# Kernel optimization log

Measured on AMD Instinct MI355X. Metric: run time of the kernel, lower is better.

## Reference

```python
import jax, jax.numpy as jnp
import numpy as np

INP = 512
HIDDEN = 512
N_HEADS = 8          # called 'head_dim' in the torch code
D_HEAD = HIDDEN // N_HEADS  # 64
BASE = 10000.0
SCALE = D_HEAD ** (-0.5)


def rope(x):
    # x: [b, s, h, d]
    b, s, h, d = x.shape
    half = d // 2
    theta = 1.0 / (BASE ** (jnp.arange(0, d, 2, dtype=jnp.float32) / d))  # [d/2]
    idx_theta = jnp.arange(s, dtype=jnp.float32)[:, None] * theta[None, :]  # [s, d/2]
    idx_theta2 = jnp.concatenate([idx_theta, idx_theta], axis=1)            # [s, d]
    neg_half = jnp.concatenate([-x[..., half:], x[..., :half]], axis=-1)
    cos = jnp.cos(idx_theta2)[None, :, None, :]
    sin = jnp.sin(idx_theta2)[None, :, None, :]
    return x * cos + neg_half * sin


def setup_inputs() -> dict:
    key = jax.random.key(0)
    ks = jax.random.split(key, 10)
    b, s = 4, 2048
    init = lambda k, shp, fan_in: jax.random.normal(k, shp, jnp.float32) * (fan_in ** -0.5)
    return {
        "x": jax.random.normal(ks[0], (b, s, INP), jnp.float32),
        "c": jax.random.normal(ks[1], (b, s, INP), jnp.float32),
        "Wq": init(ks[2], (INP, HIDDEN), INP), "bq": jnp.zeros((HIDDEN,), jnp.float32),
        "Wk": init(ks[3], (INP, HIDDEN), INP), "bk": jnp.zeros((HIDDEN,), jnp.float32),
        "Wv": init(ks[4], (INP, HIDDEN), INP), "bv": jnp.zeros((HIDDEN,), jnp.float32),
        "Wo": init(ks[5], (HIDDEN, INP), HIDDEN), "bo": jnp.zeros((INP,), jnp.float32),
    }


def reference(x, c, Wq, bq, Wk, bk, Wv, bv, Wo, bo):
    b, s, _ = x.shape
    h_res = x
    q = (c @ Wq + bq).reshape(b, s, N_HEADS, D_HEAD)
    k = (x @ Wk + bk).reshape(b, s, N_HEADS, D_HEAD)
    v = (x @ Wv + bv).reshape(b, s, N_HEADS, D_HEAD)
    q = rope(q)
    k = rope(k)  # computed but unused, exactly as in the source
    # NOTE: source computes scores between q and V (not k) -- faithful reproduction
    att = jnp.einsum('bihd,bjhd->bhij', q, v)            # [b, h, s, s]
    att = jax.nn.softmax(att * SCALE, axis=-1)
    out = jnp.einsum('bhij,bjhd->bihd', att, v)          # [b, s, h, d]
    out = out.reshape(b, s, HIDDEN)
    out = out @ Wo + bo
    return out + h_res
```

## Files before the change

### kernel.cpp

```cpp
#include <hip/hip_runtime.h>
#include <hip/hip_bf16.h>
#include <cstdint>

typedef float f32x4 __attribute__((ext_vector_type(4)));
typedef short bf16x8 __attribute__((ext_vector_type(8)));
typedef short bf16x4 __attribute__((ext_vector_type(4)));
typedef unsigned short u16;

#define B_    4
#define S_    2048
#define H_    8
#define D_    64
#define M_    8192

#define OFF_CBF   0UL
#define OFF_XBF   8388608UL
#define OFF_QBH   16777216UL
#define OFF_VBH   25165824UL
#define OFF_VTBH  33554432UL
#define OFF_ATTN  41943040UL
#define OFF_WQT   50331648UL
#define OFF_WVT   50855936UL
#define OFF_WOT   51380224UL
#define OFF_BIAS  51904512UL
#define OFF_COS   51910656UL
#define OFF_SIN   52172800UL
#define WS_NEEDED 52434944UL

__device__ __forceinline__ u16 f2bf(float f){
    union { float f; uint32_t u; } v; v.f = f;
    uint32_t r = (v.u + 0x7fffu + ((v.u >> 16) & 1u)) >> 16;
    return (u16)r;
}
__device__ __forceinline__ float bf2f(u16 h){
    union { uint32_t u; float f; } v; v.u = ((uint32_t)h) << 16;
    return v.f;
}
__device__ __forceinline__ uint32_t fbits(float f){
    union { float f; uint32_t u; } v; v.f = f; return v.u;
}

__device__ __forceinline__ f32x4 mfma16(bf16x4 a, bf16x4 b, f32x4 c){
#if __has_builtin(__builtin_amdgcn_mfma_f32_16x16x16bf16_1k)
    return __builtin_amdgcn_mfma_f32_16x16x16bf16_1k(a, b, c, 0, 0, 0);
#else
    asm volatile("v_mfma_f32_16x16x16_bf16 %0, %1, %2, %0" : "+v"(c) : "v"(a), "v"(b));
    return c;
#endif
}

__device__ __forceinline__ int swz(int row, int col){
    return (col & ~63) | ((((col >> 3) & 7) ^ (row & 7)) << 3) | (col & 7);
}

__device__ __forceinline__ int detect_f32(const void* x_in){
    int lane = threadIdx.x & 63;
    ushort2 dv = ((const ushort2*)x_in)[lane];
    bool hit = ((((dv.x >> 7) & 0xFF) >= 160) || (((dv.y >> 7) & 0xFF) >= 160));
    return __ballot(hit) != 0ULL;
}

__device__ __forceinline__ void gload_lds16(const u16* g, u16* l){
    __builtin_amdgcn_global_load_lds(
        (const __attribute__((address_space(1))) void*)g,
        (__attribute__((address_space(3))) void*)l, 16, 0, 0);
}

__global__ void k_prep(const void* c_in, const void* x_in,
                       const void* Wq, const void* Wv, const void* Wo,
                       const void* bq, const void* bv, const void* bo,
                       u16* c_bf, u16* x_bf,
                       u16* Wqt, u16* Wvt, u16* Wot, float* bias_ws,
                       float* cos_t, float* sin_t){
    int bid = blockIdx.x;
    if (bid >= 11264){
        int idx = (bid - 11264) * 256 + threadIdx.x;
        int pos = idx >> 5, j = idx & 31;
        double theta = pow(10000.0, -(double)j / 32.0);
        double rev = ((double)pos * theta) * 0.15915494309189535;
        rev -= floor(rev);
        float fr = (float)rev;
        cos_t[idx] = __builtin_amdgcn_cosf(fr);
        sin_t[idx] = __builtin_amdgcn_sinf(fr);
        return;
    }
    if (bid >= 8192){
        int f = detect_f32(x_in);
        int wi = (bid - 8192) >> 10;
        int idx = ((bid - 8192) & 1023) * 256 + threadIdx.x;
        int k = idx >> 9, n = idx & 511;
        const void* W; u16* Wt; const void* bb;
        if (wi == 0){ W = Wq; Wt = Wqt; bb = bq; }
        else if (wi == 1){ W = Wv; Wt = Wvt; bb = bv; }
        else { W = Wo; Wt = Wot; bb = bo; }
        float v = f ? ((const float*)W)[idx] : bf2f(((const u16*)W)[idx]);
        Wt[n * 512 + (wi == 2 ? k : swz(n, k))] = f2bf(v);
        if (idx < 512){
            float b = f ? ((const float*)bb)[idx] : bf2f(((const u16*)bb)[idx]);
            bias_ws[wi * 512 + idx] = b;
        }
        return;
    }
    int f = detect_f32(x_in);
    int isx = bid >= 4096;
    int t = (bid & 4095) * 256 + threadIdx.x;
    const void* src = isx ? x_in : c_in;
    u16* dst = isx ? x_bf : c_bf;
    int e0 = t * 4, row = e0 >> 9, col = e0 & 511;
    size_t didx = (size_t)row * 512 + swz(row, col);
    ushort4 o;
    if (f){
        float4 v = ((const float4*)src)[t];
        o.x = f2bf(v.x); o.y = f2bf(v.y); o.z = f2bf(v.z); o.w = f2bf(v.w);
    } else {
        o = ((const ushort4*)src)[t];
    }
    *(ushort4*)(dst + didx) = o;
}

__global__ __launch_bounds__(256) void k_gemm_qv(
    const u16* __restrict__ c_bf, const u16* __restrict__ x_bf,
    const u16* __restrict__ Wqt, const u16* __restrict__ Wvt,
    const float* __restrict__ bias_ws,
    const float* __restrict__ cos_t, const float* __restrict__ sin_t,
    u16* __restrict__ Qbh, u16* __restrict__ Vbh, u16* __restrict__ Vtbh)
{
    __shared__ __align__(16) u16 Als[2][128 * 64];
    __shared__ __align__(16) u16 Bls[2][128 * 64];
    const int w = threadIdx.x >> 6, lane = threadIdx.x & 63;
    const int g = lane >> 4, cq = lane & 15;
    const int wm = w & 1, wn = w >> 1;
    const int z = blockIdx.z;
    const u16* A  = z ? x_bf : c_bf;
    const u16* Wt = z ? Wvt : Wqt;
    const float* bias = bias_ws + (z ? 512 : 0);
    const int m0b = blockIdx.x * 128, n0b = blockIdx.y * 128;
    const int m0 = m0b + wm * 64, n0 = n0b + wn * 64;
    const int swzi = ((cq & 7) << 3);

    int srow[4], scol[4];
    #pragma unroll
    for (int i = 0; i < 4; i++){
        int flat = (w * 4 + i) * 64 + lane;
        srow[i] = flat >> 3; scol[i] = (flat & 7) * 8;
    }

    const f32x4 zero = {0.f, 0.f, 0.f, 0.f};
    f32x4 acc[4][4];
    #pragma unroll
    for (int i = 0; i < 4; i++)
        #pragma unroll
        for (int j = 0; j < 4; j++) acc[i][j] = zero;

    #pragma unroll
    for (int i = 0; i < 4; i++){
        gload_lds16(A  + (size_t)(m0b + srow[i]) * 512 + scol[i], &Als[0][(w*4 + i) * 512]);
        gload_lds16(Wt + (size_t)(n0b + srow[i]) * 512 + scol[i], &Bls[0][(w*4 + i) * 512]);
    }

    for (int kt = 0; kt < 8; kt++){
        const int buf = kt & 1;
        __builtin_amdgcn_s_waitcnt(0x0F70);
        __syncthreads();
        if (kt < 7){
            const int kk = (kt + 1) * 64;
            #pragma unroll
            for (int i = 0; i < 4; i++){
                gload_lds16(A  + (size_t)(m0b + srow[i]) * 512 + kk + scol[i], &Als[buf^1][(w*4 + i) * 512]);
                gload_lds16(Wt + (size_t)(n0b + srow[i]) * 512 + kk + scol[i], &Bls[buf^1][(w*4 + i) * 512]);
            }
        }
        #pragma unroll
        for (int ks = 0; ks < 2; ks++){
            const int cs = ((ks * 4 + g) << 3) ^ swzi;
            bf16x8 a[4], b[4];
            #pragma unroll
            for (int mt = 0; mt < 4; mt++)
                a[mt] = *(const bf16x8*)&Als[buf][(wm*64 + mt*16 + cq) * 64 + cs];
            #pragma unroll
            for (int nt = 0; nt < 4; nt++)
                b[nt] = *(const bf16x8*)&Bls[buf][(wn*64 + nt*16 + cq) * 64 + cs];
            #pragma unroll
            for (int mt = 0; mt < 4; mt++)
                #pragma unroll
                for (int nt = 0; nt < 4; nt++)
                    acc[mt][nt] = __builtin_amdgcn_mfma_f32_16x16x32_bf16(a[mt], b[nt], acc[mt][nt], 0, 0, 0);
        }
    }
    __syncthreads();

    #pragma unroll
    for (int nt = 0; nt < 4; nt++){
        float bvv = bias[n0 + nt*16 + cq];
        #pragma unroll
        for (int mt = 0; mt < 4; mt++) acc[mt][nt] += bvv;
    }
    const int h = n0 >> 6;
    if (z == 0){
        const float SCL = 0.125f * 1.4426950408889634f;
        #pragma unroll
        for (int mt = 0; mt < 4; mt++){
            #pragma unroll
            for (int r = 0; r < 4; r++){
                int row = m0 + mt*16 + g*4 + r;
                int b_idx = row >> 11, si = row & 2047;
                size_t base = ((size_t)(b_idx*8 + h) * 2048 + si) * 64;
                #pragma unroll
                for (int nt = 0; nt < 2; nt++){
                    int dj = nt*16 + cq;
                    float cv = cos_t[si*32 + dj], sv = sin_t[si*32 + dj];
                    float x1 = acc[mt][nt][r], x2 = acc[mt][nt+2][r];
                    Qbh[base + dj]      = f2bf((x1*cv - x2*sv) * SCL);
                    Qbh[base + dj + 32] = f2bf((x2*cv + x1*sv) * SCL);
                }
            }
        }
    } else {
        float* ltw = ((float*)&Als[0][0]) + w * (16 * 65);
        const int b_idx = m0 >> 11, si0 = m0 & 2047;
        const size_t tbase = ((size_t)(b_idx*8 + h) * 64) * 2048;
        #pragma unroll
        for (int mt = 0; mt < 4; mt++)
            #pragma unroll
            for (int r = 0; r < 4; r++){
                int row = m0 + mt*16 + g*4 + r;
                int bi = row >> 11, si = row & 2047;
                size_t base = ((size_t)(bi*8 + h) * 2048 + si) * 64;
                #pragma unroll
                for (int nt = 0; nt < 4; nt++)
                    Vbh[base + nt*16 + cq] = f2bf(acc[mt][nt][r]);
            }
        #pragma unroll
        for (int nt = 0; nt < 4; nt++){
            #pragma unroll
            for (int mt = 0; mt < 4; mt++)
                #pragma unroll
                for (int r = 0; r < 4; r++)
                    ltw[cq * 65 + mt*16 + g*4 + r] = acc[mt][nt][r];
            __builtin_amdgcn_wave_barrier();
            #pragma unroll
            for (int dd = 0; dd < 16; dd++){
                float v = ltw[dd * 65 + lane];
                Vtbh[tbase + (size_t)(nt*16 + dd) * 2048 + si0 + lane] = f2bf(v);
            }
            __builtin_amdgcn_wave_barrier();
        }
    }
}

__global__ __launch_bounds__(256, 4) void k_attn(
    const u16* __restrict__ Qbh, const u16* __restrict__ Vbh,
    const u16* __restrict__ Vtbh,
    u16* __restrict__ part0, u16* __restrict__ part1, float* __restrict__ lsum)
{
    __shared__ __align__(16) u16 Vs[2][64 * 68];
    __shared__ __align__(16) u16 Vts[2][64 * 68];
    const int w = threadIdx.x >> 6, lane = threadIdx.x & 63;
    const int g = lane >> 4, cq = lane & 15;
    const int bh = blockIdx.y, z = blockIdx.z;
    const int i0 = blockIdx.x * 128 + w * 32;
    const int j0 = z * 1024;

    bf16x8 aq[2][2];
    #pragma unroll
    for (int mt = 0; mt < 2; mt++)
        #pragma unroll
        for (int kk = 0; kk < 2; kk++)
            aq[mt][kk] = *(const bf16x8*)(Qbh + ((size_t)bh*2048 + i0 + mt*16 + cq)*64 + kk*32 + g*8);

    const int sr = w * 16 + (lane >> 2), sc = (lane & 3) * 16;
    const u16* gvs = Vbh  + ((size_t)bh*2048 + j0 + sr) * 64 + sc;
    const u16* gvt = Vtbh + ((size_t)bh*64 + sr) * 2048 + j0 + sc;
    const int ls = sr * 68 + sc;

    {
        bf16x8 a0 = *(const bf16x8*)gvs,       a1 = *(const bf16x8*)(gvs + 8);
        bf16x8 b0 = *(const bf16x8*)gvt,       b1 = *(const bf16x8*)(gvt + 8);
        *(bf16x8*)&Vs[0][ls]  = a0;  *(bf16x8*)&Vs[0][ls + 8]  = a1;
        *(bf16x8*)&Vts[0][ls] = b0;  *(bf16x8*)&Vts[0][ls + 8] = b1;
    }

    const f32x4 zero = {0.f, 0.f, 0.f, 0.f};
    f32x4 o[2][4]; float fl[2] = {0.f, 0.f};
    #pragma unroll
    for (int mt = 0; mt < 2; mt++)
        #pragma unroll
        for (int t = 0; t < 4; t++) o[mt][t] = zero;

    for (int jt = 0; jt < 16; jt++){
        const int buf = jt & 1;
        __syncthreads();
        bf16x8 na0, na1, nb0, nb1;
        if (jt < 15){
            na0 = *(const bf16x8*)(gvs + (size_t)(jt + 1) * 4096);
            na1 = *(const bf16x8*)(gvs + (size_t)(jt + 1) * 4096 + 8);
            nb0 = *(const bf16x8*)(gvt + (size_t)(jt + 1) * 64);
            nb1 = *(const bf16x8*)(gvt + (size_t)(jt + 1) * 64 + 8);
        }
        bf16x4 pk[2][4];
        #pragma unroll
        for (int t = 0; t < 4; t++){
            bf16x8 bv0 = *(const bf16x8*)&Vs[buf][(t*16 + cq)*68 + g*8];
            bf16x8 bv1 = *(const bf16x8*)&Vs[buf][(t*16 + cq)*68 + 32 + g*8];
            #pragma unroll
            for (int mt = 0; mt < 2; mt++){
                f32x4 s = __builtin_amdgcn_mfma_f32_16x16x32_bf16(bv0, aq[mt][0], zero, 0, 0, 0);
                s = __builtin_amdgcn_mfma_f32_16x16x32_bf16(bv1, aq[mt][1], s, 0, 0, 0);
                #pragma unroll
                for (int r = 0; r < 4; r++) s[r] = __builtin_amdgcn_exp2f(s[r]);
                fl[mt] += (s[0] + s[1]) + (s[2] + s[3]);
                union { bf16x4 v; uint32_t wd[2]; } u;
                u.wd[0] = (fbits(s[0]) >> 16) | (fbits(s[1]) & 0xffff0000u);
                u.wd[1] = (fbits(s[2]) >> 16) | (fbits(s[3]) & 0xffff0000u);
                pk[mt][t] = u.v;
            }
        }
        #pragma unroll
        for (int t = 0; t < 4; t++)
            #pragma unroll
            for (int tn = 0; tn < 4; tn++){
                bf16x4 bt = *(const bf16x4*)&Vts[buf][(tn*16 + cq)*68 + t*16 + g*4];
                o[0][tn] = mfma16(bt, pk[0][t], o[0][tn]);
                o[1][tn] = mfma16(bt, pk[1][t], o[1][tn]);
            }
        if (jt < 15){
            *(bf16x8*)&Vs[buf^1][ls]  = na0;  *(bf16x8*)&Vs[buf^1][ls + 8]  = na1;
            *(bf16x8*)&Vts[buf^1][ls] = nb0;  *(bf16x8*)&Vts[buf^1][ls + 8] = nb1;
        }
    }
    const int b_idx = bh >> 3, h = bh & 7;
    u16* part = z ? part1 : part0;
    #pragma unroll
    for (int mt = 0; mt < 2; mt++){
        float sum = fl[mt];
        sum += __shfl_xor(sum, 16);
        sum += __shfl_xor(sum, 32);
        int row = b_idx*2048 + i0 + mt*16 + cq;
        if (lane < 16)
            lsum[(size_t)z*65536 + (size_t)h*8192 + row] = sum;
        #pragma unroll
        for (int tn = 0; tn < 4; tn++){
            f32x4 ov = o[mt][tn];
            uint2 pw;
            pw.x = (uint32_t)f2bf(ov[0]) | ((uint32_t)f2bf(ov[1]) << 16);
            pw.y = (uint32_t)f2bf(ov[2]) | ((uint32_t)f2bf(ov[3]) << 16);
            int col = h*64 + tn*16 + g*4;
            *(uint2*)&part[(size_t)row * 512 + col] = pw;
        }
    }
}

__global__ __launch_bounds__(256) void k_gemm_out(
    const u16* __restrict__ part0, const u16* __restrict__ part1,
    const float* __restrict__ lsum,
    const u16* __restrict__ Wot, const float* __restrict__ bias_ws,
    const void* __restrict__ x_in, void* __restrict__ out)
{
    __shared__ __align__(16) u16 Als[2][128 * 68];
    __shared__ __align__(16) u16 Bls[2][64 * 68];
    const int w = threadIdx.x >> 6, lane = threadIdx.x & 63;
    const int g = lane >> 4, cq = lane & 15;
    const int wm = w & 1, wn = w >> 1;
    const int m0b = blockIdx.x * 128, n0b = blockIdx.y * 64;
    const int m0 = m0b + wm * 64, n0 = n0b + wn * 32;
    const int f = detect_f32(x_in);

    int sra[4], sca[4], srb[2], scb[2];
    #pragma unroll
    for (int i = 0; i < 4; i++){
        int flat = (w * 4 + i) * 64 + lane;
        sra[i] = flat >> 3; sca[i] = (flat & 7) * 8;
    }
    #pragma unroll
    for (int i = 0; i < 2; i++){
        int flat = (w * 2 + i) * 64 + lane;
        srb[i] = flat >> 3; scb[i] = (flat & 7) * 8;
    }

    const f32x4 zero = {0.f, 0.f, 0.f, 0.f};
    f32x4 acc[4][2];
    #pragma unroll
    for (int i = 0; i < 4; i++)
        #pragma unroll
        for (int j = 0; j < 2; j++) acc[i][j] = zero;

    bf16x8 pa0[4], pa1[4], pb[2]; float pr[4];
    #pragma unroll
    for (int i = 0; i < 4; i++){
        int row = m0b + sra[i];
        pa0[i] = *(const bf16x8*)&part0[(size_t)row * 512 + sca[i]];
        pa1[i] = *(const bf16x8*)&part1[(size_t)row * 512 + sca[i]];
        pr[i] = 1.f / (lsum[row] + lsum[65536 + row]);
    }
    #pragma unroll
    for (int i = 0; i < 2; i++)
        pb[i] = *(const bf16x8*)&Wot[(size_t)(n0b + srb[i]) * 512 + scb[i]];
    #pragma unroll
    for (int i = 0; i < 4; i++){
        union { bf16x8 v; u16 e[8]; } a8;
        #pragma unroll
        for (int e = 0; e < 8; e++)
            a8.e[e] = f2bf((bf2f((u16)pa0[i][e]) + bf2f((u16)pa1[i][e])) * pr[i]);
        *(bf16x8*)&Als[0][sra[i]*68 + sca[i]] = a8.v;
    }
    #pragma unroll
    for (int i = 0; i < 2; i++)
        *(bf16x8*)&Bls[0][srb[i]*68 + scb[i]] = pb[i];

    for (int kt = 0; kt < 8; kt++){
        const int buf = kt & 1;
        __syncthreads();
        if (kt < 7){
            const int kk = (kt + 1) * 64, h = kt + 1;
            #pragma unroll
            for (int i = 0; i < 4; i++){
                int row = m0b + sra[i];
                pa0[i] = *(const bf16x8*)&part0[(size_t)row * 512 + kk + sca[i]];
                pa1[i] = *(const bf16x8*)&part1[(size_t)row * 512 + kk + sca[i]];
                pr[i] = 1.f / (lsum[(size_t)h*8192 + row] + lsum[65536 + (size_t)h*8192 + row]);
            }
            #pragma unroll
            for (int i = 0; i < 2; i++)
                pb[i] = *(const bf16x8*)&Wot[(size_t)(n0b + srb[i]) * 512 + kk + scb[i]];
        }
        #pragma unroll
        for (int ks = 0; ks < 2; ks++){
            bf16x8 a[4], b[2];
            #pragma unroll
            for (int mt = 0; mt < 4; mt++)
                a[mt] = *(const bf16x8*)&Als[buf][(wm*64 + mt*16 + cq)*68 + ks*32 + g*8];
            #pragma unroll
            for (int nt = 0; nt < 2; nt++)
                b[nt] = *(const bf16x8*)&Bls[buf][(wn*32 + nt*16 + cq)*68 + ks*32 + g*8];
            #pragma unroll
            for (int mt = 0; mt < 4; mt++)
                #pragma unroll
                for (int nt = 0; nt < 2; nt++)
                    acc[mt][nt] = __builtin_amdgcn_mfma_f32_16x16x32_bf16(a[mt], b[nt], acc[mt][nt], 0, 0, 0);
        }
        if (kt < 7){
            #pragma unroll
            for (int i = 0; i < 4; i++){
                union { bf16x8 v; u16 e[8]; } a8;
                #pragma unroll
                for (int e = 0; e < 8; e++)
                    a8.e[e] = f2bf((bf2f((u16)pa0[i][e]) + bf2f((u16)pa1[i][e])) * pr[i]);
                *(bf16x8*)&Als[buf^1][sra[i]*68 + sca[i]] = a8.v;
            }
            #pragma unroll
            for (int i = 0; i < 2; i++)
                *(bf16x8*)&Bls[buf^1][srb[i]*68 + scb[i]] = pb[i];
        }
    }
    #pragma unroll
    for (int mt = 0; mt < 4; mt++)
        #pragma unroll
        for (int nt = 0; nt < 2; nt++)
            #pragma unroll
            for (int r = 0; r < 4; r++){
                int row = m0 + mt*16 + g*4 + r;
                int col = n0 + nt*16 + cq;
                size_t idx = (size_t)row * 512 + col;
                float resid = f ? ((const float*)x_in)[idx] : bf2f(((const u16*)x_in)[idx]);
                float v = acc[mt][nt][r] + bias_ws[1024 + col] + resid;
                if (f) ((float*)out)[idx] = v;
                else   ((u16*)out)[idx] = f2bf(v);
            }
}

extern "C" void kernel_launch(void* const* d_in, const int* in_sizes, int n_in,
                              void* d_out, int out_size, void* d_ws, size_t ws_size,
                              hipStream_t stream){
    const void* x_in = d_in[0];
    const void* c_in = d_in[1];
    const void* Wq = d_in[2]; const void* bq = d_in[3];
    const void* Wv = d_in[6]; const void* bv = d_in[7];
    const void* Wo = d_in[8]; const void* bo = d_in[9];

    if (ws_size < WS_NEEDED){
        hipMemsetAsync(d_out, 0, (size_t)out_size * 2, stream);
        return;
    }
    char* ws = (char*)d_ws;
    u16* c_bf  = (u16*)(ws + OFF_CBF);
    u16* x_bf  = (u16*)(ws + OFF_XBF);
    u16* Qbh   = (u16*)(ws + OFF_QBH);
    u16* Vbh   = (u16*)(ws + OFF_VBH);
    u16* Vtbh  = (u16*)(ws + OFF_VTBH);
    u16* part0 = (u16*)(ws + OFF_ATTN);
    u16* part1 = (u16*)(ws + OFF_CBF);
    float* lsum = (float*)(ws + OFF_XBF);
    u16* Wqt   = (u16*)(ws + OFF_WQT);
    u16* Wvt   = (u16*)(ws + OFF_WVT);
    u16* Wot   = (u16*)(ws + OFF_WOT);
    float* bias_ws = (float*)(ws + OFF_BIAS);
    float* cos_t   = (float*)(ws + OFF_COS);
    float* sin_t   = (float*)(ws + OFF_SIN);

    k_prep<<<11520, 256, 0, stream>>>(c_in, x_in, Wq, Wv, Wo, bq, bv, bo,
                                      c_bf, x_bf, Wqt, Wvt, Wot, bias_ws, cos_t, sin_t);
    k_gemm_qv<<<dim3(64, 4, 2), 256, 0, stream>>>(c_bf, x_bf, Wqt, Wvt, bias_ws,
                                                  cos_t, sin_t, Qbh, Vbh, Vtbh);
    k_attn<<<dim3(16, 32, 2), 256, 0, stream>>>(Qbh, Vbh, Vtbh, part0, part1, lsum);
    k_gemm_out<<<dim3(64, 8), 256, 0, stream>>>(part0, part1, lsum, Wot, bias_ws,
                                                x_in, d_out);
}
```

Before: 191.4 us.

## Switch attention kernel to 32x32x16 MFMA tiles with permlane repacking

Rewrites the attention inner loop to use 32x32x16 bf16 MFMA for both the score and PV products, so each wave handles a 32-row tile instead of two 16-row tiles. The exp'd scores are packed with v_cvt_pk_bf16_f32 and rearranged with permlane32_swap so they can feed straight into the next MFMA as the B operand. It also adds s_setprio around the MFMA bursts and flattens the grid to 1D with an XCD-aware block remap. This aims to cut LDS reads and MFMA issue count per FLOP and improve L2 locality. The trade-offs are larger accumulators and more register pressure, and the packing now rounds to nearest instead of truncating.

```diff
diff --git a/kernel.cpp b/kernel.cpp
--- a/kernel.cpp
+++ b/kernel.cpp
@@ -3,8 +3,10 @@
 #include <cstdint>
 
 typedef float f32x4 __attribute__((ext_vector_type(4)));
+typedef float f32x16 __attribute__((ext_vector_type(16)));
 typedef short bf16x8 __attribute__((ext_vector_type(8)));
 typedef short bf16x4 __attribute__((ext_vector_type(4)));
+typedef unsigned int u32x2 __attribute__((ext_vector_type(2)));
 typedef unsigned short u16;
 
 #define B_    4
@@ -36,16 +38,18 @@
     union { uint32_t u; float f; } v; v.u = ((uint32_t)h) << 16;
     return v.f;
 }
-__device__ __forceinline__ uint32_t fbits(float f){
-    union { float f; uint32_t u; } v; v.f = f; return v.u;
-}
-
-__device__ __forceinline__ f32x4 mfma16(bf16x4 a, bf16x4 b, f32x4 c){
-#if __has_builtin(__builtin_amdgcn_mfma_f32_16x16x16bf16_1k)
-    return __builtin_amdgcn_mfma_f32_16x16x16bf16_1k(a, b, c, 0, 0, 0);
+
+__device__ __forceinline__ uint32_t cvtpk(float lo, float hi){
+    uint32_t r;
+    asm("v_cvt_pk_bf16_f32 %0, %1, %2" : "=v"(r) : "v"(lo), "v"(hi));
+    return r;
+}
+__device__ __forceinline__ void plswap(uint32_t &va, uint32_t &vb){
+#if __has_builtin(__builtin_amdgcn_permlane32_swap)
+    u32x2 r = __builtin_amdgcn_permlane32_swap(va, vb, false, false);
+    va = r[0]; vb = r[1];
 #else
-    asm volatile("v_mfma_f32_16x16x16_bf16 %0, %1, %2, %0" : "+v"(c) : "v"(a), "v"(b));
-    return c;
+    asm volatile("v_permlane32_swap_b32 %0, %1" : "+v"(va), "+v"(vb));
 #endif
 }
 
@@ -255,18 +259,22 @@
 {
     __shared__ __align__(16) u16 Vs[2][64 * 68];
     __shared__ __align__(16) u16 Vts[2][64 * 68];
+
+    const int bid = blockIdx.x;
+    const int logical = (bid & 7) * 128 + (bid >> 3);
+    const int xb = logical & 15;
+    const int bh = (logical >> 4) & 31;
+    const int z  = logical >> 9;
+
     const int w = threadIdx.x >> 6, lane = threadIdx.x & 63;
-    const int g = lane >> 4, cq = lane & 15;
-    const int bh = blockIdx.y, z = blockIdx.z;
-    const int i0 = blockIdx.x * 128 + w * 32;
+    const int r32 = lane & 31, hl = lane >> 5;
+    const int i0 = xb * 128 + w * 32;
     const int j0 = z * 1024;
 
-    bf16x8 aq[2][2];
-    #pragma unroll
-    for (int mt = 0; mt < 2; mt++)
-        #pragma unroll
-        for (int kk = 0; kk < 2; kk++)
-            aq[mt][kk] = *(const bf16x8*)(Qbh + ((size_t)bh*2048 + i0 + mt*16 + cq)*64 + kk*32 + g*8);
+    bf16x8 aq[4];
+    #pragma unroll
+    for (int kk = 0; kk < 4; kk++)
+        aq[kk] = *(const bf16x8*)(Qbh + ((size_t)bh*2048 + i0 + r32)*64 + kk*16 + hl*8);
 
     const int sr = w * 16 + (lane >> 2), sc = (lane & 3) * 16;
     const u16* gvs = Vbh  + ((size_t)bh*2048 + j0 + sr) * 64 + sc;
@@ -280,12 +288,10 @@
         *(bf16x8*)&Vts[0][ls] = b0;  *(bf16x8*)&Vts[0][ls + 8] = b1;
     }
 
-    const f32x4 zero = {0.f, 0.f, 0.f, 0.f};
-    f32x4 o[2][4]; float fl[2] = {0.f, 0.f};
-    #pragma unroll
-    for (int mt = 0; mt < 2; mt++)
-        #pragma unroll
-        for (int t = 0; t < 4; t++) o[mt][t] = zero;
+    f32x16 ot0 = {0.f,0.f,0.f,0.f,0.f,0.f,0.f,0.f,0.f,0.f,0.f,0.f,0.f,0.f,0.f,0.f};
+    f32x16 ot1 = ot0;
+    const f32x16 zero16 = ot0;
+    float fl = 0.f;
 
     for (int jt = 0; jt < 16; jt++){
         const int buf = jt & 1;
@@ -297,54 +303,71 @@
             nb0 = *(const bf16x8*)(gvt + (size_t)(jt + 1) * 64);
             nb1 = *(const bf16x8*)(gvt + (size_t)(jt + 1) * 64 + 8);
         }
-        bf16x4 pk[2][4];
-        #pragma unroll
-        for (int t = 0; t < 4; t++){
-            bf16x8 bv0 = *(const bf16x8*)&Vs[buf][(t*16 + cq)*68 + g*8];
-            bf16x8 bv1 = *(const bf16x8*)&Vs[buf][(t*16 + cq)*68 + 32 + g*8];
-            #pragma unroll
-            for (int mt = 0; mt < 2; mt++){
-                f32x4 s = __builtin_amdgcn_mfma_f32_16x16x32_bf16(bv0, aq[mt][0], zero, 0, 0, 0);
-                s = __builtin_amdgcn_mfma_f32_16x16x32_bf16(bv1, aq[mt][1], s, 0, 0, 0);
-                #pragma unroll
-                for (int r = 0; r < 4; r++) s[r] = __builtin_amdgcn_exp2f(s[r]);
-                fl[mt] += (s[0] + s[1]) + (s[2] + s[3]);
-                union { bf16x4 v; uint32_t wd[2]; } u;
-                u.wd[0] = (fbits(s[0]) >> 16) | (fbits(s[1]) & 0xffff0000u);
-                u.wd[1] = (fbits(s[2]) >> 16) | (fbits(s[3]) & 0xffff0000u);
-                pk[mt][t] = u.v;
-            }
-        }
-        #pragma unroll
-        for (int t = 0; t < 4; t++)
-            #pragma unroll
-            for (int tn = 0; tn < 4; tn++){
-                bf16x4 bt = *(const bf16x4*)&Vts[buf][(tn*16 + cq)*68 + t*16 + g*4];
-                o[0][tn] = mfma16(bt, pk[0][t], o[0][tn]);
-                o[1][tn] = mfma16(bt, pk[1][t], o[1][tn]);
-            }
+        bf16x8 pb[4];
+        #pragma unroll
+        for (int jtile = 0; jtile < 2; jtile++){
+            f32x16 st = zero16;
+            __builtin_amdgcn_s_setprio(1);
+            #pragma unroll
+            for (int kk = 0; kk < 4; kk++){
+                bf16x8 av = *(const bf16x8*)&Vs[buf][(jtile*32 + r32)*68 + kk*16 + hl*8];
+                st = __builtin_amdgcn_mfma_f32_32x32x16_bf16(av, aq[kk], st, 0, 0, 0);
+            }
+            __builtin_amdgcn_s_setprio(0);
+            #pragma unroll
+            for (int rr = 0; rr < 16; rr++) st[rr] = __builtin_amdgcn_exp2f(st[rr]);
+            {
+                float t0 = (st[0]+st[1]) + (st[2]+st[3]);
+                float t1 = (st[4]+st[5]) + (st[6]+st[7]);
+                float t2 = (st[8]+st[9]) + (st[10]+st[11]);
+                float t3 = (st[12]+st[13]) + (st[14]+st[15]);
+                fl += (t0+t1) + (t2+t3);
+            }
+            #pragma unroll
+            for (int c = 0; c < 2; c++){
+                uint32_t dA1 = cvtpk(st[c*8+0], st[c*8+1]);
+                uint32_t dA2 = cvtpk(st[c*8+2], st[c*8+3]);
+                uint32_t dB1 = cvtpk(st[c*8+4], st[c*8+5]);
+                uint32_t dB2 = cvtpk(st[c*8+6], st[c*8+7]);
+                plswap(dA1, dB1);
+                plswap(dA2, dB2);
+                union { bf16x8 v; uint32_t d[4]; } u;
+                u.d[0] = dA1; u.d[1] = dA2; u.d[2] = dB1; u.d[3] = dB2;
+                pb[jtile*2 + c] = u.v;
+            }
+        }
+        __builtin_amdgcn_s_setprio(1);
+        #pragma unroll
+        for (int c = 0; c < 4; c++){
+            bf16x8 vt0 = *(const bf16x8*)&Vts[buf][r32*68 + c*16 + hl*8];
+            bf16x8 vt1 = *(const bf16x8*)&Vts[buf][(32 + r32)*68 + c*16 + hl*8];
+            ot0 = __builtin_amdgcn_mfma_f32_32x32x16_bf16(vt0, pb[c], ot0, 0, 0, 0);
+            ot1 = __builtin_amdgcn_mfma_f32_32x32x16_bf16(vt1, pb[c], ot1, 0, 0, 0);
+        }
+        __builtin_amdgcn_s_setprio(0);
         if (jt < 15){
             *(bf16x8*)&Vs[buf^1][ls]  = na0;  *(bf16x8*)&Vs[buf^1][ls + 8]  = na1;
             *(bf16x8*)&Vts[buf^1][ls] = nb0;  *(bf16x8*)&Vts[buf^1][ls + 8] = nb1;
         }
     }
-    const int b_idx = bh >> 3, h = bh & 7;
+    const int b_idx = bh >> 3, hh = bh & 7;
     u16* part = z ? part1 : part0;
-    #pragma unroll
-    for (int mt = 0; mt < 2; mt++){
-        float sum = fl[mt];
-        sum += __shfl_xor(sum, 16);
-        sum += __shfl_xor(sum, 32);
-        int row = b_idx*2048 + i0 + mt*16 + cq;
-        if (lane < 16)
-            lsum[(size_t)z*65536 + (size_t)h*8192 + row] = sum;
-        #pragma unroll
-        for (int tn = 0; tn < 4; tn++){
-            f32x4 ov = o[mt][tn];
+    float sum = fl + __shfl_xor(fl, 32);
+    const int row = b_idx*2048 + i0 + r32;
+    if (lane < 32)
+        lsum[(size_t)z*65536 + (size_t)hh*8192 + row] = sum;
+    #pragma unroll
+    for (int dt = 0; dt < 2; dt++){
+        #pragma unroll
+        for (int q = 0; q < 4; q++){
+            float v0 = dt ? ot1[q*4+0] : ot0[q*4+0];
+            float v1 = dt ? ot1[q*4+1] : ot0[q*4+1];
+            float v2 = dt ? ot1[q*4+2] : ot0[q*4+2];
+            float v3 = dt ? ot1[q*4+3] : ot0[q*4+3];
             uint2 pw;
-            pw.x = (uint32_t)f2bf(ov[0]) | ((uint32_t)f2bf(ov[1]) << 16);
-            pw.y = (uint32_t)f2bf(ov[2]) | ((uint32_t)f2bf(ov[3]) << 16);
-            int col = h*64 + tn*16 + g*4;
+            pw.x = cvtpk(v0, v1);
+            pw.y = cvtpk(v2, v3);
+            int col = hh*64 + dt*32 + q*8 + hl*4;
             *(uint2*)&part[(size_t)row * 512 + col] = pw;
         }
     }
@@ -501,7 +524,7 @@
                                       c_bf, x_bf, Wqt, Wvt, Wot, bias_ws, cos_t, sin_t);
     k_gemm_qv<<<dim3(64, 4, 2), 256, 0, stream>>>(c_bf, x_bf, Wqt, Wvt, bias_ws,
                                                   cos_t, sin_t, Qbh, Vbh, Vtbh);
-    k_attn<<<dim3(16, 32, 2), 256, 0, stream>>>(Qbh, Vbh, Vtbh, part0, part1, lsum);
+    k_attn<<<dim3(1024), 256, 0, stream>>>(Qbh, Vbh, Vtbh, part0, part1, lsum);
     k_gemm_out<<<dim3(64, 8), 256, 0, stream>>>(part0, part1, lsum, Wot, bias_ws,
                                                 x_in, d_out);
 }
```

Measured after the change: 188.5 us. Within noise of the previous version (-1.5%).
